# Kernel optimization log

Hardware: AMD Instinct MI355X
Metric: run time of the kernel (lower is better)

## Reference

```python
import jax, jax.numpy as jnp
import numpy as np

D_MODEL = 2048
NUM_EXPERTS = 64
TOP_K = 2
ALPHA = 0.01


def setup_inputs() -> dict:
    key = jax.random.key(0)
    kx, kw = jax.random.split(key)
    x = jax.random.normal(kx, (4, 4096, D_MODEL), dtype=jnp.float32)
    # kaiming-uniform-ish gate weight, bound = 1/sqrt(d_model)
    bound = 1.0 / np.sqrt(D_MODEL)
    W = jax.random.uniform(kw, (NUM_EXPERTS, D_MODEL), dtype=jnp.float32,
                           minval=-bound, maxval=bound)
    return {"x": x, "W": W}


def reference(x, W):
    bsz, seq, h = x.shape
    xf = x.reshape(-1, h)                       # [N, h], N = bsz*seq
    logits = xf @ W.T                            # [N, E]
    scores = jax.nn.softmax(logits, axis=-1)     # [N, E]
    topk_weight, topk_idx = jax.lax.top_k(scores, TOP_K)  # [N, k], [N, k]
    if TOP_K > 1:
        topk_weight = topk_weight / (topk_weight.sum(axis=-1, keepdims=True) + 1e-9)
    # aux loss (training path, alpha > 0)
    one_hot = jax.nn.one_hot(topk_idx.reshape(-1), NUM_EXPERTS, dtype=jnp.float32)
    freq = one_hot.mean(axis=0)                  # [E]
    Pi = scores.mean(axis=0)                     # [E]
    fi = freq * NUM_EXPERTS
    aux_loss = (Pi * fi).sum() * ALPHA
    return topk_weight, topk_idx, aux_loss
```

## Files before the change

kernel.cpp:

```cpp
#include <hip/hip_runtime.h>
#include <math.h>
#include <stdint.h>


#define D_MODEL 2048
#define NE      64
#define N_ROWS  16384
#define ALPHA   0.01f
#define BR      32
#define BK      64
#define NCH     (D_MODEL / BK)
#define THREADS 512

typedef _Float16 f16x8 __attribute__((ext_vector_type(8)));
typedef float    f32x4 __attribute__((ext_vector_type(4)));

union U4 { uint32_t u[4]; uint4 v; };
union F8 { uint32_t u[4]; f16x8 v; };

__device__ __forceinline__ uint32_t pack_hl(float xs) {
    _Float16 h = (_Float16)xs;
    float hf = (float)h;
    _Float16 l = (_Float16)(xs - hf);
    union { _Float16 f; uint16_t b; } ch, cl;
    ch.f = h; cl.f = l;
    return (uint32_t)ch.b | ((uint32_t)cl.b << 16);
}

#define GLD16(src, dst) __builtin_amdgcn_global_load_lds( \
    (const __attribute__((address_space(1))) void*)(src), \
    (__attribute__((address_space(3))) void*)(dst), 16, 0, 0)

__global__ __launch_bounds__(256)
void w_prep(const float* __restrict__ W, uint32_t* __restrict__ img) {
    const int idx = blockIdx.x * 256 + threadIdx.x;
    const int e = idx >> 11, k = idx & 2047;
    const uint32_t u = pack_hl(W[idx] * 1024.0f);
    const int c = k >> 6, kl = k & 63, su = kl >> 2, d = kl & 3;
    img[(size_t)c * 4096 + (e * 16 + (su ^ (e & 7))) * 4 + d] = u;
}

__global__ __launch_bounds__(THREADS, 4)
void router_mfma(const float* __restrict__ x, const uint32_t* __restrict__ wimg,
                 float* __restrict__ out_w, float* __restrict__ out_i,
                 float* __restrict__ g_pi, float* __restrict__ g_cnt) {
    __shared__ __align__(16) uint32_t sm[2 * 2048 + 2 * 4096];
    __shared__ float apx[8][NE], acn[8][NE];

    uint32_t* lx = sm;
    uint32_t* lw = sm + 4096;
    float*    ll = (float*)sm;

    const int tid  = threadIdx.x;
    const int lane = tid & 63;
    const int wv   = tid >> 6;
    const int rb   = blockIdx.x * BR;

    const int srow = tid >> 4;
    const int ssu  = tid & 15;
    const float* xg = x + (size_t)(rb + srow) * D_MODEL + ssu * 4;
    const int xw_off = (srow * 16 + (ssu ^ (srow & 7))) * 4;

    const int mt = wv >> 2, nt = wv & 3;
    const int arow = mt * 16 + (lane & 15);
    const int be   = nt * 16 + (lane & 15);
    const int kq   = lane >> 4;
    const int ap = arow & 7, bp = be & 7;

    f32x4 acc = {0.f, 0.f, 0.f, 0.f};

    {
        const float4 p0 = *(const float4*)xg;
        uint4 w0;
        w0.x = pack_hl(p0.x * 256.f); w0.y = pack_hl(p0.y * 256.f);
        w0.z = pack_hl(p0.z * 256.f); w0.w = pack_hl(p0.w * 256.f);
        *(uint4*)(lx + xw_off) = w0;
        GLD16(wimg + (size_t)tid * 4,         lw + tid * 4);
        GLD16(wimg + (size_t)(tid + 512) * 4, lw + (tid + 512) * 4);
    }
    float4 px = *(const float4*)(xg + BK);
    __syncthreads();

    for (int t = 0; t < NCH; ++t) {
        const int buf = t & 1, nbuf = buf ^ 1;

        if (t + 1 < NCH) {
            const uint32_t* ws = wimg + (size_t)(t + 1) * 4096;
            GLD16(ws + (size_t)tid * 4,         lw + nbuf * 4096 + tid * 4);
            GLD16(ws + (size_t)(tid + 512) * 4, lw + nbuf * 4096 + (tid + 512) * 4);
        }

        const uint32_t* lxb = lx + buf * 2048;
        const uint32_t* lwb = lw + buf * 4096;
        #pragma unroll
        for (int ks = 0; ks < 2; ++ks) {
            const int su0 = ks * 8 + kq * 2;
            U4 a0, a1, b0, b1;
            a0.v = *(const uint4*)(lxb + (arow * 16 + ( su0      ^ ap)) * 4);
            a1.v = *(const uint4*)(lxb + (arow * 16 + ((su0 + 1) ^ ap)) * 4);
            b0.v = *(const uint4*)(lwb + (be   * 16 + ( su0      ^ bp)) * 4);
            b1.v = *(const uint4*)(lwb + (be   * 16 + ((su0 + 1) ^ bp)) * 4);
            F8 ah, al, bh, bl;
            #pragma unroll
            for (int p = 0; p < 2; ++p) {
                ah.u[p]     = __builtin_amdgcn_perm(a0.u[2*p+1], a0.u[2*p], 0x05040100u);
                al.u[p]     = __builtin_amdgcn_perm(a0.u[2*p+1], a0.u[2*p], 0x07060302u);
                ah.u[2 + p] = __builtin_amdgcn_perm(a1.u[2*p+1], a1.u[2*p], 0x05040100u);
                al.u[2 + p] = __builtin_amdgcn_perm(a1.u[2*p+1], a1.u[2*p], 0x07060302u);
                bh.u[p]     = __builtin_amdgcn_perm(b0.u[2*p+1], b0.u[2*p], 0x05040100u);
                bl.u[p]     = __builtin_amdgcn_perm(b0.u[2*p+1], b0.u[2*p], 0x07060302u);
                bh.u[2 + p] = __builtin_amdgcn_perm(b1.u[2*p+1], b1.u[2*p], 0x05040100u);
                bl.u[2 + p] = __builtin_amdgcn_perm(b1.u[2*p+1], b1.u[2*p], 0x07060302u);
            }
            acc = __builtin_amdgcn_mfma_f32_16x16x32_f16(ah.v, bh.v, acc, 0, 0, 0);
            acc = __builtin_amdgcn_mfma_f32_16x16x32_f16(ah.v, bl.v, acc, 0, 0, 0);
            acc = __builtin_amdgcn_mfma_f32_16x16x32_f16(al.v, bh.v, acc, 0, 0, 0);
        }

        if (t + 1 < NCH) {
            uint4 wo;
            wo.x = pack_hl(px.x * 256.f); wo.y = pack_hl(px.y * 256.f);
            wo.z = pack_hl(px.z * 256.f); wo.w = pack_hl(px.w * 256.f);
            *(uint4*)(lx + nbuf * 2048 + xw_off) = wo;
            if (t + 2 < NCH) px = *(const float4*)(xg + (size_t)(t + 2) * BK);
        }
        __syncthreads();
    }

    #pragma unroll
    for (int r = 0; r < 4; ++r) {
        const int row = mt * 16 + kq * 4 + r;
        ll[row * 68 + be] = acc[r] * (1.0f / 262144.0f);
    }
    __syncthreads();

    float pi_acc = 0.f, cnt_acc = 0.f;
    for (int rr = 0; rr < 4; ++rr) {
        const int row = wv * 4 + rr;
        const float lg = ll[row * 68 + lane];

        float m = lg;
        #pragma unroll
        for (int off = 32; off; off >>= 1) m = fmaxf(m, __shfl_xor(m, off));
        const float e = expf(lg - m);
        float s = e;
        #pragma unroll
        for (int off = 32; off; off >>= 1) s += __shfl_xor(s, off);
        const float score = e / s;

        float v1 = score; int i1 = lane;
        #pragma unroll
        for (int off = 32; off; off >>= 1) {
            const float ov = __shfl_xor(v1, off);
            const int   oi = __shfl_xor(i1, off);
            if (ov > v1 || (ov == v1 && oi < i1)) { v1 = ov; i1 = oi; }
        }
        float v2 = (lane == i1) ? -1.f : score; int i2 = lane;
        #pragma unroll
        for (int off = 32; off; off >>= 1) {
            const float ov = __shfl_xor(v2, off);
            const int   oi = __shfl_xor(i2, off);
            if (ov > v2 || (ov == v2 && oi < i2)) { v2 = ov; i2 = oi; }
        }

        if (lane == 0) {
            const int grow = rb + row;
            const float denom = v1 + v2 + 1e-9f;
            out_w[grow * 2 + 0] = v1 / denom;
            out_w[grow * 2 + 1] = v2 / denom;
            out_i[grow * 2 + 0] = (float)i1;
            out_i[grow * 2 + 1] = (float)i2;
        }
        pi_acc  += score;
        cnt_acc += (float)((lane == i1) + (lane == i2));
    }

    apx[wv][lane] = pi_acc;
    acn[wv][lane] = cnt_acc;
    __syncthreads();

    if (tid < NE) {
        float p = 0.f, c = 0.f;
        #pragma unroll
        for (int w = 0; w < 8; ++w) { p += apx[w][tid]; c += acn[w][tid]; }
        atomicAdd(&g_pi[tid],  p);
        atomicAdd(&g_cnt[tid], c);
    }
}

__global__ void router_finalize(const float* __restrict__ g_pi,
                                const float* __restrict__ g_cnt,
                                float* __restrict__ aux_out) {
    const int lane = threadIdx.x;
    const float pi = g_pi[lane] * (1.0f / (float)N_ROWS);
    const float fi = g_cnt[lane] * (64.0f / (float)(N_ROWS * 2));
    float v = pi * fi;
    #pragma unroll
    for (int off = 32; off; off >>= 1) v += __shfl_xor(v, off);
    if (lane == 0) aux_out[0] = v * ALPHA;
}

extern "C" void kernel_launch(void* const* d_in, const int* in_sizes, int n_in,
                              void* d_out, int out_size, void* d_ws, size_t ws_size,
                              hipStream_t stream) {
    const float* x = (const float*)d_in[0];
    const float* W = (const float*)d_in[1];

    float* out   = (float*)d_out;
    float* out_w = out;
    float* out_i = out + N_ROWS * 2;
    float* aux   = out + N_ROWS * 4;

    float*    g_pi  = (float*)d_ws;
    float*    g_cnt = g_pi + NE;
    uint32_t* wimg  = (uint32_t*)d_ws + 256;

    hipMemsetAsync(d_ws, 0, 512, stream);

    w_prep<<<dim3(512), dim3(256), 0, stream>>>(W, wimg);
    router_mfma<<<dim3(N_ROWS / BR), dim3(THREADS), 0, stream>>>(
        x, wimg, out_w, out_i, g_pi, g_cnt);
    router_finalize<<<dim3(1), dim3(64), 0, stream>>>(g_pi, g_cnt, aux);
}
```

Before: 218.3 us.

## Pre-split W into fp16 hi/lo planes and relax barrier waits to keep x prefetch in flight

The weight-prep kernel now writes separate hi and lo fp16 planes for each 64-wide K chunk, with a matching swizzle. The main loop can then load the B fragments directly as f16x8 vectors instead of unpacking them with perm instructions. The per-iteration __syncthreads is replaced by an explicit s_waitcnt vmcnt(1) plus s_barrier, so the global load that prefetches the next x chunk stays outstanding across the barrier while the LDS weight loads complete. This relies on exact ordering of memory operations for correctness, and a full wait is kept on the final iterations.

```diff
diff --git a/kernel.cpp b/kernel.cpp
--- a/kernel.cpp
+++ b/kernel.cpp
@@ -31,13 +31,30 @@
     (const __attribute__((address_space(1))) void*)(src), \
     (__attribute__((address_space(3))) void*)(dst), 16, 0, 0)
 
+#define BAR_KEEP1() { asm volatile("s_waitcnt vmcnt(1) lgkmcnt(0)" ::: "memory"); \
+                      __builtin_amdgcn_s_barrier(); \
+                      __builtin_amdgcn_sched_barrier(0); }
+#define BAR_FULL()  { asm volatile("s_waitcnt vmcnt(0) lgkmcnt(0)" ::: "memory"); \
+                      __builtin_amdgcn_s_barrier(); \
+                      __builtin_amdgcn_sched_barrier(0); }
+
 __global__ __launch_bounds__(256)
 void w_prep(const float* __restrict__ W, uint32_t* __restrict__ img) {
     const int idx = blockIdx.x * 256 + threadIdx.x;
-    const int e = idx >> 11, k = idx & 2047;
-    const uint32_t u = pack_hl(W[idx] * 1024.0f);
-    const int c = k >> 6, kl = k & 63, su = kl >> 2, d = kl & 3;
-    img[(size_t)c * 4096 + (e * 16 + (su ^ (e & 7))) * 4 + d] = u;
+    const int e = idx >> 10, kp = (idx & 1023) * 2;
+    const float w0 = W[(size_t)e * D_MODEL + kp]     * 1024.0f;
+    const float w1 = W[(size_t)e * D_MODEL + kp + 1] * 1024.0f;
+    _Float16 h0 = (_Float16)w0; _Float16 l0 = (_Float16)(w0 - (float)h0);
+    _Float16 h1 = (_Float16)w1; _Float16 l1 = (_Float16)(w1 - (float)h1);
+    union { _Float16 f[2]; uint32_t u; } ph, pl;
+    ph.f[0] = h0; ph.f[1] = h1;
+    pl.f[0] = l0; pl.f[1] = l1;
+    const int c = kp >> 6, kl = kp & 63;
+    const int slot = kl >> 3, uo = (kl & 7) >> 1;
+    const int so = (e * 8 + (slot ^ (e & 7))) * 4 + uo;
+    uint32_t* base = img + (size_t)c * 4096;
+    base[so]        = ph.u;
+    base[2048 + so] = pl.u;
 }
 
 __global__ __launch_bounds__(THREADS, 4)
@@ -79,7 +96,7 @@
         GLD16(wimg + (size_t)(tid + 512) * 4, lw + (tid + 512) * 4);
     }
     float4 px = *(const float4*)(xg + BK);
-    __syncthreads();
+    BAR_KEEP1();
 
     for (int t = 0; t < NCH; ++t) {
         const int buf = t & 1, nbuf = buf ^ 1;
@@ -95,22 +112,20 @@
         #pragma unroll
         for (int ks = 0; ks < 2; ++ks) {
             const int su0 = ks * 8 + kq * 2;
-            U4 a0, a1, b0, b1;
+            const int sb  = ks * 4 + kq;
+            U4 a0, a1;
             a0.v = *(const uint4*)(lxb + (arow * 16 + ( su0      ^ ap)) * 4);
             a1.v = *(const uint4*)(lxb + (arow * 16 + ((su0 + 1) ^ ap)) * 4);
-            b0.v = *(const uint4*)(lwb + (be   * 16 + ( su0      ^ bp)) * 4);
-            b1.v = *(const uint4*)(lwb + (be   * 16 + ((su0 + 1) ^ bp)) * 4);
-            F8 ah, al, bh, bl;
+            F8 bh, bl;
+            bh.v = *(const f16x8*)(lwb +        (be * 8 + (sb ^ bp)) * 4);
+            bl.v = *(const f16x8*)(lwb + 2048 + (be * 8 + (sb ^ bp)) * 4);
+            F8 ah, al;
             #pragma unroll
             for (int p = 0; p < 2; ++p) {
                 ah.u[p]     = __builtin_amdgcn_perm(a0.u[2*p+1], a0.u[2*p], 0x05040100u);
                 al.u[p]     = __builtin_amdgcn_perm(a0.u[2*p+1], a0.u[2*p], 0x07060302u);
                 ah.u[2 + p] = __builtin_amdgcn_perm(a1.u[2*p+1], a1.u[2*p], 0x05040100u);
                 al.u[2 + p] = __builtin_amdgcn_perm(a1.u[2*p+1], a1.u[2*p], 0x07060302u);
-                bh.u[p]     = __builtin_amdgcn_perm(b0.u[2*p+1], b0.u[2*p], 0x05040100u);
-                bl.u[p]     = __builtin_amdgcn_perm(b0.u[2*p+1], b0.u[2*p], 0x07060302u);
-                bh.u[2 + p] = __builtin_amdgcn_perm(b1.u[2*p+1], b1.u[2*p], 0x05040100u);
-                bl.u[2 + p] = __builtin_amdgcn_perm(b1.u[2*p+1], b1.u[2*p], 0x07060302u);
             }
             acc = __builtin_amdgcn_mfma_f32_16x16x32_f16(ah.v, bh.v, acc, 0, 0, 0);
             acc = __builtin_amdgcn_mfma_f32_16x16x32_f16(ah.v, bl.v, acc, 0, 0, 0);
@@ -124,7 +139,8 @@
             *(uint4*)(lx + nbuf * 2048 + xw_off) = wo;
             if (t + 2 < NCH) px = *(const float4*)(xg + (size_t)(t + 2) * BK);
         }
-        __syncthreads();
+
+        if (t + 2 < NCH) { BAR_KEEP1(); } else { BAR_FULL(); }
     }
 
     #pragma unroll
@@ -217,7 +233,7 @@
 
     hipMemsetAsync(d_ws, 0, 512, stream);
 
-    w_prep<<<dim3(512), dim3(256), 0, stream>>>(W, wimg);
+    w_prep<<<dim3(256), dim3(256), 0, stream>>>(W, wimg);
     router_mfma<<<dim3(N_ROWS / BR), dim3(THREADS), 0, stream>>>(
         x, wimg, out_w, out_i, g_pi, g_cnt);
     router_finalize<<<dim3(1), dim3(64), 0, stream>>>(g_pi, g_cnt, aux);
```

Result: no change. 218.2 us (-0.1%).
